# Optimization experiments

Measured on AMD Instinct MI355X. Metric: run time of the kernel, lower is better.

Reference implementation:

```python
import jax, jax.numpy as jnp
import numpy as np

EPS = 0.1        # entropic regularization epsilon
MAX_ITER = 15    # fixed number of Sinkhorn iterations (no early stop for determinism)
TINY = 1e-16     # denominator stabilizer, matches torch code
NORM_EPS = 1e-8  # cosine-norm clamp, matches torch code


def setup_inputs() -> dict:
    key = jax.random.key(0)
    k1, k2 = jax.random.split(key)
    x = jax.random.normal(k1, (32, 512, 256), dtype=jnp.float32)
    y = jax.random.normal(k2, (32, 512, 256), dtype=jnp.float32)
    return {"x": x, "y": y}


def _cosine_distance(x, y):
    # C[b,n,m] = 1 - <x_n, y_m> / max(|x_n||y_m|, eps)
    w1 = jnp.linalg.norm(x, axis=-1, keepdims=True)            # [b,n,1]
    w2 = jnp.linalg.norm(y, axis=-1, keepdims=True)            # [b,m,1]
    dots = jnp.einsum('bnd,bmd->bnm', x, y)                    # [b,n,m]
    denom = jnp.maximum(w1 * jnp.swapaxes(w2, -2, -1), NORM_EPS)
    return 1.0 - dots / denom


def _sinkhorn(C):
    nb, n, m = C.shape
    # uniform marginals (a=None, b=None in the torch module); mask is all ones
    a = jnp.full((nb, n), 1.0 / n, dtype=C.dtype)
    b = jnp.full((nb, m), 1.0 / m, dtype=C.dtype)

    def log_K(alpha, beta):
        # log K = (-C + alpha 1^T + 1 beta^T) / eps
        return (-C + alpha[:, :, None] + beta[:, None, :]) / EPS

    def step(carry, _):
        u, v, alpha, beta = carry
        K = jnp.exp(log_K(alpha, beta))
        u = a / (jnp.einsum('bnm,bm->bn', K, v) + TINY)   # K v
        v = b / (jnp.einsum('bnm,bn->bm', K, u) + TINY)   # K^T u
        alpha = alpha + EPS * jnp.log(u)  # absorb u into log scaling
        beta = beta + EPS * jnp.log(v)    # absorb v into log scaling
        return (u, v, alpha, beta), None

    init = (jnp.ones((nb, n), C.dtype), jnp.ones((nb, m), C.dtype),
            jnp.zeros((nb, n), C.dtype), jnp.zeros((nb, m), C.dtype))
    (u, v, alpha, beta), _ = jax.lax.scan(step, init, None, length=MAX_ITER)

    # P = exp(log u + log K + log v) with the FINAL alpha/beta (as in torch code)
    pi = jnp.exp(jnp.log(u)[:, :, None] + log_K(alpha, beta) + jnp.log(v)[:, None, :])
    cost = jnp.sum(pi * C, axis=(-2, -1))  # reduction='none' -> per-batch cost [nb]
    return cost, pi, C


def reference(x, y):
    C = _cosine_distance(x, y)
    return _sinkhorn(C)
```

## Files before the change

### kernel.cpp

```cpp
#include <hip/hip_runtime.h>
#include <hip/hip_fp16.h>
#include <math.h>

#define NB 32
#define NN 512
#define DD 256
#define NROW  (NB*NN)
#define NELEM (NB*NN*DD)

constexpr float INV_EPS   = 10.0f;
constexpr float F_TINY    = 1e-16f;
constexpr float F_NORMEPS = 1e-8f;
constexpr float MARG      = 1.0f / 512.0f;

#define BARS_N 2112

typedef __attribute__((ext_vector_type(8))) short bf16x8;
typedef __attribute__((ext_vector_type(4))) float f32x4;

__device__ __forceinline__ unsigned short f2bf(float f) {
    unsigned u = __float_as_uint(f);
    u += 0x7fffu + ((u >> 16) & 1u);
    return (unsigned short)(u >> 16);
}

__global__ __launch_bounds__(256) void norms_convert(
        const float* __restrict__ x, const float* __restrict__ y,
        float* __restrict__ nx, float* __restrict__ ny,
        unsigned short* __restrict__ xh, unsigned short* __restrict__ yh,
        float* __restrict__ cost, int* __restrict__ bars) {
    if (blockIdx.x == 0) {
        if (threadIdx.x < NB) cost[threadIdx.x] = 0.0f;
        for (int i = threadIdx.x; i < BARS_N; i += 256) bars[i] = 0;
    }
    int w = threadIdx.x >> 6, l = threadIdx.x & 63;
    int row = blockIdx.x * 4 + w;
    bool isx = row < NROW;
    int r = isx ? row : row - NROW;
    const float* src = (isx ? x : y) + (size_t)r * DD;
    float4 v = ((const float4*)src)[l];
    float ss = v.x * v.x + v.y * v.y + v.z * v.z + v.w * v.w;
#pragma unroll
    for (int off = 32; off; off >>= 1) ss += __shfl_xor(ss, off);

    unsigned short* ph = (isx ? xh : yh) + (size_t)r * DD + l * 4;
    *(ushort4*)ph = make_ushort4(f2bf(v.x), f2bf(v.y), f2bf(v.z), f2bf(v.w));
    if (l == 0) (isx ? nx : ny)[r] = sqrtf(ss);
}

__global__ __launch_bounds__(256) void gemm_cos_mfma(
        const unsigned short* __restrict__ xh, const unsigned short* __restrict__ yh,
        const float* __restrict__ nx, const float* __restrict__ ny,
        float* __restrict__ C, __half* __restrict__ Ef) {
    int blk = blockIdx.x;
    int b = blk >> 4, ti = (blk >> 2) & 3, tj = blk & 3;
    __shared__ short Ah[128][32], Bh[128][32];
    const unsigned short* xbh = xh + ((size_t)b * NN + ti * 128) * DD;
    const unsigned short* ybh = yh + ((size_t)b * NN + tj * 128) * DD;
    int t = threadIdx.x, w = t >> 6, l = t & 63;
    int rw = w * 32, q = l >> 4, low = l & 15;

    f32x4 acc[2][8];
#pragma unroll
    for (int i = 0; i < 2; ++i)
#pragma unroll
        for (int j = 0; j < 8; ++j) acc[i][j] = (f32x4){0.f, 0.f, 0.f, 0.f};

    int sr = t >> 1, h = t & 1;
    int c0i = 2 * h, c1i = 2 * h + 1;
    int sw0 = (c0i ^ ((sr >> 1) & 3)) * 8;
    int sw1 = (c1i ^ ((sr >> 1) & 3)) * 8;

    for (int k0 = 0; k0 < DD; k0 += 32) {
        {
            const int4* ga = (const int4*)(xbh + (size_t)sr * DD + k0);
            const int4* gc = (const int4*)(ybh + (size_t)sr * DD + k0);
            int4 a0 = ga[c0i], a1 = ga[c1i];
            int4 c0 = gc[c0i], c1 = gc[c1i];
            *(int4*)&Ah[sr][sw0] = a0; *(int4*)&Ah[sr][sw1] = a1;
            *(int4*)&Bh[sr][sw0] = c0; *(int4*)&Bh[sr][sw1] = c1;
        }
        __syncthreads();

        bf16x8 ah[2];
#pragma unroll
        for (int ti2 = 0; ti2 < 2; ++ti2) {
            int m = rw + ti2 * 16 + low;
            int pq = (q ^ ((m >> 1) & 3)) * 8;
            ah[ti2] = *(const bf16x8*)&Ah[m][pq];
        }
#pragma unroll
        for (int tj2 = 0; tj2 < 8; ++tj2) {
            int n = tj2 * 16 + low;
            int pq = (q ^ ((n >> 1) & 3)) * 8;
            bf16x8 bh = *(const bf16x8*)&Bh[n][pq];
#pragma unroll
            for (int ti2 = 0; ti2 < 2; ++ti2)
                acc[ti2][tj2] = __builtin_amdgcn_mfma_f32_16x16x32_bf16(
                    ah[ti2], bh, acc[ti2][tj2], 0, 0, 0);
        }
        __syncthreads();
    }

    float*  Cb = C  + (size_t)b * NN * NN;
    __half* Eb = Ef + (size_t)b * NN * NN;
#pragma unroll
    for (int ti2 = 0; ti2 < 2; ++ti2) {
#pragma unroll
        for (int tj2 = 0; tj2 < 8; ++tj2) {
            int gm0 = ti * 128 + rw + ti2 * 16 + q * 4;
            int gn  = tj * 128 + tj2 * 16 + low;
            float nyc = ny[b * NN + gn];
            f32x4 a = acc[ti2][tj2];
#pragma unroll
            for (int reg = 0; reg < 4; ++reg) {
                int gm = gm0 + reg;
                float d = 1.0f - a[reg] / fmaxf(nx[b * NN + gm] * nyc, F_NORMEPS);
                Cb[(size_t)gm * NN + gn] = d;
                Eb[(size_t)gm * NN + gn] = __float2half(__expf(-INV_EPS * d));
            }
        }
    }
}

__global__ __launch_bounds__(512, 2) void sink_fused(
        const __half* __restrict__ Ef, const float* __restrict__ C,
        float* __restrict__ cp0, float* __restrict__ cp1,
        float* __restrict__ pi, float* __restrict__ cost,
        int* __restrict__ bars) {
    int blk = blockIdx.x;
    int xcd = blk & 7, qq = blk >> 3;
    int o = qq & 7;
    int b = ((qq >> 3) << 3) | xcd;
    int blkbase = blk - 8 * o;
    int tt = threadIdx.x, w = tt >> 6, l = tt & 63;
    int* bcnt = &bars[b * 64];
    int* brel = &bars[b * 64 + 16];
    int* gcnt = &bars[2048];

    __shared__ __half sE[64][NN];
    __shared__ float sW[NN];
    __shared__ float sWP[8][NN];
    __shared__ float sPart[8];

    {
        const __half* Eb = Ef + ((size_t)b * NN + o * 64 + w * 8) * NN + 8 * l;
#pragma unroll
        for (int i = 0; i < 8; ++i) {
            int4 raw = *(const int4*)(Eb + (size_t)i * NN);
            *(int4*)&sE[w * 8 + i][8 * l] = raw;
        }
    }

    float A[8], Pr[8];
#pragma unroll
    for (int i = 0; i < 8; ++i) { A[i] = 1.0f; Pr[i] = 0.0f; }
    float Br = 1.0f;

    float* cpr = cp0;
    float* cpw = cp1;

    for (int t = 1; t <= 15; ++t) {
        if (t == 1) {
            sW[tt] = 1.0f;
        } else {
            float sv = 0.0f;
#pragma unroll
            for (int k = 0; k < 8; ++k)
                sv += __hip_atomic_load(
                    &cpr[(size_t)(blkbase + 8 * k) * NN + tt],
                    __ATOMIC_RELAXED, __HIP_MEMORY_SCOPE_AGENT);
            float vv = MARG / (Br * sv + F_TINY);
            Br *= vv;
            sW[tt] = Br * vv;
        }
        __syncthreads();

        int4 raw[8];
#pragma unroll
        for (int i = 0; i < 8; ++i)
            raw[i] = *(const int4*)&sE[w * 8 + i][8 * l];

        float wr[8];
        *(float4*)&wr[0] = *(const float4*)&sW[8 * l];
        *(float4*)&wr[4] = *(const float4*)&sW[8 * l + 4];

#pragma unroll
        for (int i = 0; i < 8; ++i) {
            const __half* hv = (const __half*)&raw[i];
            float s = 0.0f;
#pragma unroll
            for (int e = 0; e < 8; ++e) s = fmaf(__half2float(hv[e]), wr[e], s);
#pragma unroll
            for (int off = 32; off; off >>= 1) s += __shfl_xor(s, off);
            float uu = MARG / (A[i] * s + F_TINY);
            A[i] *= uu;
            if (t == 15) Pr[i] = A[i] * uu;
        }

        float p[8];
#pragma unroll
        for (int e = 0; e < 8; ++e) p[e] = 0.0f;
#pragma unroll
        for (int i = 0; i < 8; ++i) {
            const __half* hv = (const __half*)&raw[i];
#pragma unroll
            for (int e = 0; e < 8; ++e)
                p[e] = fmaf(__half2float(hv[e]), A[i], p[e]);
        }
        *(float4*)&sWP[w][8 * l]     = make_float4(p[0], p[1], p[2], p[3]);
        *(float4*)&sWP[w][8 * l + 4] = make_float4(p[4], p[5], p[6], p[7]);
        __syncthreads();
        float cs = 0.0f;
#pragma unroll
        for (int ww = 0; ww < 8; ++ww) cs += sWP[ww][tt];
        cpw[(size_t)blk * NN + tt] = cs;

        __syncthreads();
        if (tt == 0) {
            __hip_atomic_fetch_add(bcnt, 1, __ATOMIC_RELAXED,
                                   __HIP_MEMORY_SCOPE_AGENT);
            while (__hip_atomic_load(bcnt, __ATOMIC_RELAXED,
                                     __HIP_MEMORY_SCOPE_AGENT) < 8 * t)
                __builtin_amdgcn_s_sleep(1);
        }
        __syncthreads();

        float* tmp = cpr; cpr = cpw; cpw = tmp;
    }

    {
        float sv = 0.0f;
#pragma unroll
        for (int k = 0; k < 8; ++k)
            sv += __hip_atomic_load(
                &cpr[(size_t)(blkbase + 8 * k) * NN + tt],
                __ATOMIC_RELAXED, __HIP_MEMORY_SCOPE_AGENT);
        float vv = MARG / (Br * sv + F_TINY);
        sW[tt] = Br * vv * vv;
    }

    __syncthreads();
    if (tt == 0) {
        __hip_atomic_fetch_add(bcnt, 1, __ATOMIC_RELAXED,
                               __HIP_MEMORY_SCOPE_AGENT);
        if (o == 0) {
            while (__hip_atomic_load(bcnt, __ATOMIC_RELAXED,
                                     __HIP_MEMORY_SCOPE_AGENT) < 128)
                __builtin_amdgcn_s_sleep(1);
            __hip_atomic_fetch_add(gcnt, 1, __ATOMIC_RELAXED,
                                   __HIP_MEMORY_SCOPE_AGENT);
            while (__hip_atomic_load(gcnt, __ATOMIC_RELAXED,
                                     __HIP_MEMORY_SCOPE_AGENT) < 32)
                __builtin_amdgcn_s_sleep(1);
            __hip_atomic_store(brel, 1, __ATOMIC_RELAXED,
                               __HIP_MEMORY_SCOPE_AGENT);
        } else {
            while (__hip_atomic_load(brel, __ATOMIC_RELAXED,
                                     __HIP_MEMORY_SCOPE_AGENT) == 0)
                __builtin_amdgcn_s_sleep(1);
        }
    }
    __syncthreads();

    float q0[8];
    *(float4*)&q0[0] = *(const float4*)&sW[4 * l];
    *(float4*)&q0[4] = *(const float4*)&sW[256 + 4 * l];
    const float* Cb = C + (size_t)b * NN * NN;
    float* pib = pi + (size_t)b * NN * NN;
    float csum = 0.0f;
#pragma unroll 1
    for (int i = 0; i < 8; ++i) {
        int r = o * 64 + w * 8 + i;
        float pf = Pr[i];
        const float* crow = Cb + (size_t)r * NN;
        float* prow = pib + (size_t)r * NN;
        float4 c0 = *(const float4*)(crow + 4 * l);
        float4 c1 = *(const float4*)(crow + 256 + 4 * l);
        float pv0 = pf * q0[0] * __expf(-INV_EPS * c0.x);
        float pv1 = pf * q0[1] * __expf(-INV_EPS * c0.y);
        float pv2 = pf * q0[2] * __expf(-INV_EPS * c0.z);
        float pv3 = pf * q0[3] * __expf(-INV_EPS * c0.w);
        float pv4 = pf * q0[4] * __expf(-INV_EPS * c1.x);
        float pv5 = pf * q0[5] * __expf(-INV_EPS * c1.y);
        float pv6 = pf * q0[6] * __expf(-INV_EPS * c1.z);
        float pv7 = pf * q0[7] * __expf(-INV_EPS * c1.w);
        *(float4*)(prow + 4 * l)       = make_float4(pv0, pv1, pv2, pv3);
        *(float4*)(prow + 256 + 4 * l) = make_float4(pv4, pv5, pv6, pv7);
        csum = fmaf(pv0, c0.x, csum); csum = fmaf(pv1, c0.y, csum);
        csum = fmaf(pv2, c0.z, csum); csum = fmaf(pv3, c0.w, csum);
        csum = fmaf(pv4, c1.x, csum); csum = fmaf(pv5, c1.y, csum);
        csum = fmaf(pv6, c1.z, csum); csum = fmaf(pv7, c1.w, csum);
    }
#pragma unroll
    for (int off = 32; off; off >>= 1) csum += __shfl_xor(csum, off);
    if (l == 0) sPart[w] = csum;
    __syncthreads();
    if (tt == 0) {
        float tot = 0.0f;
#pragma unroll
        for (int ww = 0; ww < 8; ++ww) tot += sPart[ww];
        atomicAdd(&cost[b], tot);
    }
}

extern "C" void kernel_launch(void* const* d_in, const int* in_sizes, int n_in,
                              void* d_out, int out_size, void* d_ws, size_t ws_size,
                              hipStream_t stream) {
    const float* x = (const float*)d_in[0];
    const float* y = (const float*)d_in[1];
    float* out  = (float*)d_out;
    float* cost = out;
    float* pi   = out + 32;
    float* C    = out + 32 + (size_t)NB * NN * NN;

    float* ws = (float*)d_ws;
    float* nx = ws;
    float* ny = ws + 16384;
    int* bars = (int*)(ws + 32768);

    unsigned short* xh = (unsigned short*)pi;
    unsigned short* yh = xh + NELEM;
    __half* Ef = (__half*)(yh + NELEM);
    float* cp0 = pi;
    float* cp1 = pi + 256 * NN;

    norms_convert<<<dim3(8192), dim3(256), 0, stream>>>(
        x, y, nx, ny, xh, yh, cost, bars);
    gemm_cos_mfma<<<dim3(512), dim3(256), 0, stream>>>(
        xh, yh, nx, ny, C, Ef);

    const __half* Ef_p = Ef; const float* C_p = C;
    float* cp0_p = cp0; float* cp1_p = cp1;
    float* pi_p = pi; float* cost_p = cost; int* bars_p = bars;
    void* args[] = { &Ef_p, &C_p, &cp0_p, &cp1_p, &pi_p, &cost_p, &bars_p };
    hipLaunchCooperativeKernel(reinterpret_cast<void*>(sink_fused),
                               dim3(256), dim3(512), args, 0, stream);
}
```

Measured before the change: 188.0 us.

## Interleave two batches per block to hide per-batch Sinkhorn barrier latency

Each cooperative block now owns 32 rows from each of two batches instead of 64 rows from one, and alternates between them within each iteration. While one batch's barrier is pending, the block works on the other batch, so spin-wait latency on the per-batch counters is meant to overlap with useful compute. Each batch is now split across 16 blocks instead of 8, so the column-partial reduction reads 16 partials per column, and the count thresholds and partial-buffer layout are adjusted to match. This adds more global partial traffic and more block-level syncs per iteration.

```diff
diff --git a/kernel.cpp b/kernel.cpp
--- a/kernel.cpp
+++ b/kernel.cpp
@@ -129,178 +129,213 @@
         float* __restrict__ pi, float* __restrict__ cost,
         int* __restrict__ bars) {
     int blk = blockIdx.x;
-    int xcd = blk & 7, qq = blk >> 3;
-    int o = qq & 7;
-    int b = ((qq >> 3) << 3) | xcd;
-    int blkbase = blk - 8 * o;
+    int xcd = blk & 7, j = blk >> 3;
+    int o = j & 15;
+    int p = j >> 4;
+    int b1 = xcd + 16 * p;
+    int b2 = b1 + 8;
     int tt = threadIdx.x, w = tt >> 6, l = tt & 63;
-    int* bcnt = &bars[b * 64];
-    int* brel = &bars[b * 64 + 16];
     int* gcnt = &bars[2048];
 
-    __shared__ __half sE[64][NN];
+    __shared__ __half sE[2][32][NN];
     __shared__ float sW[NN];
     __shared__ float sWP[8][NN];
+    __shared__ float sQ[2][NN];
     __shared__ float sPart[8];
 
-    {
-        const __half* Eb = Ef + ((size_t)b * NN + o * 64 + w * 8) * NN + 8 * l;
-#pragma unroll
-        for (int i = 0; i < 8; ++i) {
+#pragma unroll
+    for (int s = 0; s < 2; ++s) {
+        int bb = s ? b2 : b1;
+        const __half* Eb = Ef + ((size_t)bb * NN + o * 32 + w * 4) * NN + 8 * l;
+#pragma unroll
+        for (int i = 0; i < 4; ++i) {
             int4 raw = *(const int4*)(Eb + (size_t)i * NN);
-            *(int4*)&sE[w * 8 + i][8 * l] = raw;
-        }
-    }
-
-    float A[8], Pr[8];
-#pragma unroll
-    for (int i = 0; i < 8; ++i) { A[i] = 1.0f; Pr[i] = 0.0f; }
-    float Br = 1.0f;
+            *(int4*)&sE[s][w * 4 + i][8 * l] = raw;
+        }
+    }
+
+    float Br[2] = { 1.0f, 1.0f };
+    float A[2][4], Pr[2][4];
+#pragma unroll
+    for (int s = 0; s < 2; ++s)
+#pragma unroll
+        for (int i = 0; i < 4; ++i) { A[s][i] = 1.0f; Pr[s][i] = 0.0f; }
 
     float* cpr = cp0;
     float* cpw = cp1;
 
     for (int t = 1; t <= 15; ++t) {
-        if (t == 1) {
-            sW[tt] = 1.0f;
-        } else {
-            float sv = 0.0f;
-#pragma unroll
-            for (int k = 0; k < 8; ++k)
-                sv += __hip_atomic_load(
-                    &cpr[(size_t)(blkbase + 8 * k) * NN + tt],
-                    __ATOMIC_RELAXED, __HIP_MEMORY_SCOPE_AGENT);
-            float vv = MARG / (Br * sv + F_TINY);
-            Br *= vv;
-            sW[tt] = Br * vv;
-        }
-        __syncthreads();
-
-        int4 raw[8];
-#pragma unroll
-        for (int i = 0; i < 8; ++i)
-            raw[i] = *(const int4*)&sE[w * 8 + i][8 * l];
-
-        float wr[8];
-        *(float4*)&wr[0] = *(const float4*)&sW[8 * l];
-        *(float4*)&wr[4] = *(const float4*)&sW[8 * l + 4];
-
-#pragma unroll
-        for (int i = 0; i < 8; ++i) {
-            const __half* hv = (const __half*)&raw[i];
-            float s = 0.0f;
-#pragma unroll
-            for (int e = 0; e < 8; ++e) s = fmaf(__half2float(hv[e]), wr[e], s);
-#pragma unroll
-            for (int off = 32; off; off >>= 1) s += __shfl_xor(s, off);
-            float uu = MARG / (A[i] * s + F_TINY);
-            A[i] *= uu;
-            if (t == 15) Pr[i] = A[i] * uu;
-        }
-
-        float p[8];
-#pragma unroll
-        for (int e = 0; e < 8; ++e) p[e] = 0.0f;
-#pragma unroll
-        for (int i = 0; i < 8; ++i) {
-            const __half* hv = (const __half*)&raw[i];
-#pragma unroll
-            for (int e = 0; e < 8; ++e)
-                p[e] = fmaf(__half2float(hv[e]), A[i], p[e]);
-        }
-        *(float4*)&sWP[w][8 * l]     = make_float4(p[0], p[1], p[2], p[3]);
-        *(float4*)&sWP[w][8 * l + 4] = make_float4(p[4], p[5], p[6], p[7]);
-        __syncthreads();
-        float cs = 0.0f;
-#pragma unroll
-        for (int ww = 0; ww < 8; ++ww) cs += sWP[ww][tt];
-        cpw[(size_t)blk * NN + tt] = cs;
-
-        __syncthreads();
-        if (tt == 0) {
-            __hip_atomic_fetch_add(bcnt, 1, __ATOMIC_RELAXED,
-                                   __HIP_MEMORY_SCOPE_AGENT);
-            while (__hip_atomic_load(bcnt, __ATOMIC_RELAXED,
-                                     __HIP_MEMORY_SCOPE_AGENT) < 8 * t)
-                __builtin_amdgcn_s_sleep(1);
-        }
-        __syncthreads();
-
+#pragma unroll
+        for (int s = 0; s < 2; ++s) {
+            int bb = s ? b2 : b1;
+            int* bcnt = &bars[bb * 64];
+
+            if (t > 1) {
+                if (tt == 0) {
+                    while (__hip_atomic_load(bcnt, __ATOMIC_RELAXED,
+                                             __HIP_MEMORY_SCOPE_AGENT) < 16 * (t - 1))
+                        __builtin_amdgcn_s_sleep(1);
+                }
+                __syncthreads();
+            }
+
+            if (t == 1) {
+                sW[tt] = 1.0f;
+            } else {
+                float sv = 0.0f;
+#pragma unroll
+                for (int k = 0; k < 16; ++k)
+                    sv += __hip_atomic_load(
+                        &cpr[(size_t)(bb * 16 + k) * NN + tt],
+                        __ATOMIC_RELAXED, __HIP_MEMORY_SCOPE_AGENT);
+                float vv = MARG / (Br[s] * sv + F_TINY);
+                Br[s] *= vv;
+                sW[tt] = Br[s] * vv;
+            }
+            __syncthreads();
+
+            int4 raw[4];
+#pragma unroll
+            for (int i = 0; i < 4; ++i)
+                raw[i] = *(const int4*)&sE[s][w * 4 + i][8 * l];
+            float wr[8];
+            *(float4*)&wr[0] = *(const float4*)&sW[8 * l];
+            *(float4*)&wr[4] = *(const float4*)&sW[8 * l + 4];
+
+#pragma unroll
+            for (int i = 0; i < 4; ++i) {
+                const __half* hv = (const __half*)&raw[i];
+                float sacc = 0.0f;
+#pragma unroll
+                for (int e = 0; e < 8; ++e)
+                    sacc = fmaf(__half2float(hv[e]), wr[e], sacc);
+#pragma unroll
+                for (int off = 32; off; off >>= 1) sacc += __shfl_xor(sacc, off);
+                float uu = MARG / (A[s][i] * sacc + F_TINY);
+                A[s][i] *= uu;
+                if (t == 15) Pr[s][i] = A[s][i] * uu;
+            }
+
+            float pp[8];
+#pragma unroll
+            for (int e = 0; e < 8; ++e) pp[e] = 0.0f;
+#pragma unroll
+            for (int i = 0; i < 4; ++i) {
+                const __half* hv = (const __half*)&raw[i];
+#pragma unroll
+                for (int e = 0; e < 8; ++e)
+                    pp[e] = fmaf(__half2float(hv[e]), A[s][i], pp[e]);
+            }
+            *(float4*)&sWP[w][8 * l]     = make_float4(pp[0], pp[1], pp[2], pp[3]);
+            *(float4*)&sWP[w][8 * l + 4] = make_float4(pp[4], pp[5], pp[6], pp[7]);
+            __syncthreads();
+            float cs = 0.0f;
+#pragma unroll
+            for (int ww = 0; ww < 8; ++ww) cs += sWP[ww][tt];
+            cpw[(size_t)(bb * 16 + o) * NN + tt] = cs;
+
+            __syncthreads();
+            if (tt == 0)
+                __hip_atomic_fetch_add(bcnt, 1, __ATOMIC_RELAXED,
+                                       __HIP_MEMORY_SCOPE_AGENT);
+        }
         float* tmp = cpr; cpr = cpw; cpw = tmp;
     }
 
-    {
+    if (tt == 0) {
+        int* bc = &bars[b1 * 64];
+        while (__hip_atomic_load(bc, __ATOMIC_RELAXED,
+                                 __HIP_MEMORY_SCOPE_AGENT) < 240)
+            __builtin_amdgcn_s_sleep(1);
+    } else if (tt == 1) {
+        int* bc = &bars[b2 * 64];
+        while (__hip_atomic_load(bc, __ATOMIC_RELAXED,
+                                 __HIP_MEMORY_SCOPE_AGENT) < 240)
+            __builtin_amdgcn_s_sleep(1);
+    }
+    __syncthreads();
+#pragma unroll
+    for (int s = 0; s < 2; ++s) {
+        int bb = s ? b2 : b1;
         float sv = 0.0f;
 #pragma unroll
-        for (int k = 0; k < 8; ++k)
+        for (int k = 0; k < 16; ++k)
             sv += __hip_atomic_load(
-                &cpr[(size_t)(blkbase + 8 * k) * NN + tt],
+                &cpr[(size_t)(bb * 16 + k) * NN + tt],
                 __ATOMIC_RELAXED, __HIP_MEMORY_SCOPE_AGENT);
-        float vv = MARG / (Br * sv + F_TINY);
-        sW[tt] = Br * vv * vv;
+        float vv = MARG / (Br[s] * sv + F_TINY);
+        sQ[s][tt] = Br[s] * vv * vv;
     }
 
     __syncthreads();
-    if (tt == 0) {
-        __hip_atomic_fetch_add(bcnt, 1, __ATOMIC_RELAXED,
+    if (tt < 2) {
+        int bb = tt ? b2 : b1;
+        int* bc  = &bars[bb * 64];
+        int* brl = &bars[bb * 64 + 16];
+        __hip_atomic_fetch_add(bc, 1, __ATOMIC_RELAXED,
                                __HIP_MEMORY_SCOPE_AGENT);
         if (o == 0) {
-            while (__hip_atomic_load(bcnt, __ATOMIC_RELAXED,
-                                     __HIP_MEMORY_SCOPE_AGENT) < 128)
+            while (__hip_atomic_load(bc, __ATOMIC_RELAXED,
+                                     __HIP_MEMORY_SCOPE_AGENT) < 256)
                 __builtin_amdgcn_s_sleep(1);
             __hip_atomic_fetch_add(gcnt, 1, __ATOMIC_RELAXED,
                                    __HIP_MEMORY_SCOPE_AGENT);
             while (__hip_atomic_load(gcnt, __ATOMIC_RELAXED,
                                      __HIP_MEMORY_SCOPE_AGENT) < 32)
                 __builtin_amdgcn_s_sleep(1);
-            __hip_atomic_store(brel, 1, __ATOMIC_RELAXED,
+            __hip_atomic_store(brl, 1, __ATOMIC_RELAXED,
                                __HIP_MEMORY_SCOPE_AGENT);
         } else {
-            while (__hip_atomic_load(brel, __ATOMIC_RELAXED,
+            while (__hip_atomic_load(brl, __ATOMIC_RELAXED,
                                      __HIP_MEMORY_SCOPE_AGENT) == 0)
                 __builtin_amdgcn_s_sleep(1);
         }
     }
     __syncthreads();
 
-    float q0[8];
-    *(float4*)&q0[0] = *(const float4*)&sW[4 * l];
-    *(float4*)&q0[4] = *(const float4*)&sW[256 + 4 * l];
-    const float* Cb = C + (size_t)b * NN * NN;
-    float* pib = pi + (size_t)b * NN * NN;
-    float csum = 0.0f;
+#pragma unroll
+    for (int s = 0; s < 2; ++s) {
+        int bb = s ? b2 : b1;
+        float q0[8];
+        *(float4*)&q0[0] = *(const float4*)&sQ[s][4 * l];
+        *(float4*)&q0[4] = *(const float4*)&sQ[s][256 + 4 * l];
+        const float* Cb = C + (size_t)bb * NN * NN;
+        float* pib = pi + (size_t)bb * NN * NN;
+        float csum = 0.0f;
 #pragma unroll 1
-    for (int i = 0; i < 8; ++i) {
-        int r = o * 64 + w * 8 + i;
-        float pf = Pr[i];
-        const float* crow = Cb + (size_t)r * NN;
-        float* prow = pib + (size_t)r * NN;
-        float4 c0 = *(const float4*)(crow + 4 * l);
-        float4 c1 = *(const float4*)(crow + 256 + 4 * l);
-        float pv0 = pf * q0[0] * __expf(-INV_EPS * c0.x);
-        float pv1 = pf * q0[1] * __expf(-INV_EPS * c0.y);
-        float pv2 = pf * q0[2] * __expf(-INV_EPS * c0.z);
-        float pv3 = pf * q0[3] * __expf(-INV_EPS * c0.w);
-        float pv4 = pf * q0[4] * __expf(-INV_EPS * c1.x);
-        float pv5 = pf * q0[5] * __expf(-INV_EPS * c1.y);
-        float pv6 = pf * q0[6] * __expf(-INV_EPS * c1.z);
-        float pv7 = pf * q0[7] * __expf(-INV_EPS * c1.w);
-        *(float4*)(prow + 4 * l)       = make_float4(pv0, pv1, pv2, pv3);
-        *(float4*)(prow + 256 + 4 * l) = make_float4(pv4, pv5, pv6, pv7);
-        csum = fmaf(pv0, c0.x, csum); csum = fmaf(pv1, c0.y, csum);
-        csum = fmaf(pv2, c0.z, csum); csum = fmaf(pv3, c0.w, csum);
-        csum = fmaf(pv4, c1.x, csum); csum = fmaf(pv5, c1.y, csum);
-        csum = fmaf(pv6, c1.z, csum); csum = fmaf(pv7, c1.w, csum);
-    }
-#pragma unroll
-    for (int off = 32; off; off >>= 1) csum += __shfl_xor(csum, off);
-    if (l == 0) sPart[w] = csum;
-    __syncthreads();
-    if (tt == 0) {
-        float tot = 0.0f;
-#pragma unroll
-        for (int ww = 0; ww < 8; ++ww) tot += sPart[ww];
-        atomicAdd(&cost[b], tot);
+        for (int i = 0; i < 4; ++i) {
+            int r = o * 32 + w * 4 + i;
+            float pf = Pr[s][i];
+            const float* crow = Cb + (size_t)r * NN;
+            float* prow = pib + (size_t)r * NN;
+            float4 c0 = *(const float4*)(crow + 4 * l);
+            float4 c1 = *(const float4*)(crow + 256 + 4 * l);
+            float pv0 = pf * q0[0] * __expf(-INV_EPS * c0.x);
+            float pv1 = pf * q0[1] * __expf(-INV_EPS * c0.y);
+            float pv2 = pf * q0[2] * __expf(-INV_EPS * c0.z);
+            float pv3 = pf * q0[3] * __expf(-INV_EPS * c0.w);
+            float pv4 = pf * q0[4] * __expf(-INV_EPS * c1.x);
+            float pv5 = pf * q0[5] * __expf(-INV_EPS * c1.y);
+            float pv6 = pf * q0[6] * __expf(-INV_EPS * c1.z);
+            float pv7 = pf * q0[7] * __expf(-INV_EPS * c1.w);
+            *(float4*)(prow + 4 * l)       = make_float4(pv0, pv1, pv2, pv3);
+            *(float4*)(prow + 256 + 4 * l) = make_float4(pv4, pv5, pv6, pv7);
+            csum = fmaf(pv0, c0.x, csum); csum = fmaf(pv1, c0.y, csum);
+            csum = fmaf(pv2, c0.z, csum); csum = fmaf(pv3, c0.w, csum);
+            csum = fmaf(pv4, c1.x, csum); csum = fmaf(pv5, c1.y, csum);
+            csum = fmaf(pv6, c1.z, csum); csum = fmaf(pv7, c1.w, csum);
+        }
+#pragma unroll
+        for (int off = 32; off; off >>= 1) csum += __shfl_xor(csum, off);
+        if (l == 0) sPart[w] = csum;
+        __syncthreads();
+        if (tt == 0) {
+            float tot = 0.0f;
+#pragma unroll
+            for (int ww = 0; ww < 8; ++ww) tot += sPart[ww];
+            atomicAdd(&cost[bb], tot);
+        }
+        __syncthreads();
     }
 }
 
@@ -323,7 +358,7 @@
     unsigned short* yh = xh + NELEM;
     __half* Ef = (__half*)(yh + NELEM);
     float* cp0 = pi;
-    float* cp1 = pi + 256 * NN;
+    float* cp1 = pi + (size_t)NB * 16 * NN;
 
     norms_convert<<<dim3(8192), dim3(256), 0, stream>>>(
         x, y, nx, ny, xh, yh, cost, bars);
```

Result: slower. 217.6 us (+15.7%).
